# Kernel tuning notes

Measured on AMD Instinct MI355X. Metric: run time of the kernel, lower is better.

Reference implementation:

```python
import jax, jax.numpy as jnp
import numpy as np
from jax import lax

K = 5          # kernel_size
P = K // 2     # padding
DN = ('NCHW', 'OIHW', 'NCHW')


def _dwconv(z, wt, bt):
    # depthwise conv: z [b,c,h,w], wt [c,1,K,K], bt [c]
    c = z.shape[1]
    y = lax.conv_general_dilated(z, wt, (1, 1), [(P, P), (P, P)],
                                 feature_group_count=c, dimension_numbers=DN)
    return y + bt[None, :, None, None]


def setup_inputs() -> dict:
    key = jax.random.key(0)
    ks = jax.random.split(key, 8)
    b, c, h, w = 8, 64, 256, 256
    return {
        'x': jax.random.normal(ks[0], (b, c, h, w), jnp.float32),
        'w1': jax.random.normal(ks[1], (3, c, 1, K, K), jnp.float32) * 0.1,
        'b1': jax.random.normal(ks[2], (3, c), jnp.float32) * 0.1,
        'w2': jax.random.normal(ks[3], (3, c, 1, K, K), jnp.float32) * 0.1,
        'b2': jax.random.normal(ks[4], (3, c), jnp.float32) * 0.1,
        'wk': jax.random.normal(ks[5], (K * K * c, c), jnp.float32) * 0.1,
        'bk': jax.random.normal(ks[6], (K * K * c,), jnp.float32) * 0.1,
        'bias': jnp.zeros((c,), jnp.float32),
    }


def reference(x, w1, b1, w2, b2, wk, bk, bias):
    b, c, h, w = x.shape
    # avgpool 2x2 stride 2
    t = x.reshape(b, c, h // 2, 2, w // 2, 2).mean(axis=(3, 5))
    # Block1: 3 depthwise convs
    for i in range(3):
        t = _dwconv(t, w1[i], b1[i])
    # maxpool 2x2 stride 2
    hh, ww = t.shape[2], t.shape[3]
    t = t.reshape(b, c, hh // 2, 2, ww // 2, 2).max(axis=(3, 5))
    # Block2: 3 depthwise convs
    for i in range(3):
        t = _dwconv(t, w2[i], b2[i])
    # adaptive avg pool to 1x1 -> [b, c]
    g = t.mean(axis=(2, 3))
    # tokernel 1x1 conv -> per-sample depthwise kernels [b*c, 1, K, K]
    kern = (jnp.einsum('bc,oc->bo', g, wk) + bk).reshape(b * c, 1, K, K)
    # per-sample dynamic depthwise conv (groups = b*c)
    y = lax.conv_general_dilated(x.reshape(1, b * c, h, w), kern, (1, 1),
                                 [(P, P), (P, P)], feature_group_count=b * c,
                                 dimension_numbers=DN)
    return y.reshape(b, c, h, w) + bias[None, :, None, None]
```

## Files before the change

### kernel.cpp

```cpp
#include <hip/hip_runtime.h>

#define BB 8
#define CC 64
#define HH 256
#define WW 256
#define H1 128
#define W1 128
#define KK 5

template<int SS>
__device__ __forceinline__ void conv4x4(const float* __restrict__ src,
                                        const float* __restrict__ wr,
                                        float bv, float a[4][4])
{
#pragma unroll
    for (int i = 0; i < 4; i++)
#pragma unroll
        for (int j = 0; j < 4; j++) a[i][j] = bv;
#pragma unroll
    for (int ir = 0; ir < 8; ir++) {
        const float* s = src + ir * SS;
        float4 L = *(const float4*)s;
        float4 R = *(const float4*)(s + 4);
        float e[8] = {L.x, L.y, L.z, L.w, R.x, R.y, R.z, R.w};
#pragma unroll
        for (int i = 0; i < 4; i++) {
            const int ky = ir - i;
            if (ky >= 0 && ky < 5) {
#pragma unroll
                for (int kx = 0; kx < 5; kx++) {
                    const float wv = wr[ky * 5 + kx];
#pragma unroll
                    for (int j = 0; j < 4; j++) a[i][j] += e[j + kx] * wv;
                }
            }
        }
    }
}

__global__ __launch_bounds__(512, 4) void k_block1(
    const float* __restrict__ x, const float* __restrict__ w1,
    const float* __restrict__ b1, float* __restrict__ t1)
{
    const int plane = blockIdx.z;
    const int c = plane & 63;
    const int tx = blockIdx.x, ty = blockIdx.y;
    const int tid = threadIdx.x;

    __shared__ __align__(16) float sA[76 * 76];
    __shared__ __align__(16) float sB[72 * 76];

    const float* xp = x + (size_t)plane * HH * WW;
    const int row0 = ty * 64 - 6, col0 = tx * 64 - 6;

    for (int i = tid; i < 76 * 38; i += 512) {
        int r = i / 38, j = i % 38;
        int gr = row0 + r;
        int xc = 2 * col0 + 4 * j;
        float4 t0 = make_float4(0.f, 0.f, 0.f, 0.f);
        float4 t1v = make_float4(0.f, 0.f, 0.f, 0.f);
        if ((unsigned)gr < H1 && (unsigned)xc < WW) {
            t0  = *(const float4*)(xp + (size_t)(2 * gr) * WW + xc);
            t1v = *(const float4*)(xp + (size_t)(2 * gr + 1) * WW + xc);
        }
        float p0 = 0.25f * (t0.x + t0.y + t1v.x + t1v.y);
        float p1 = 0.25f * (t0.z + t0.w + t1v.z + t1v.w);
        *(float2*)&sA[r * 76 + 2 * j] = make_float2(p0, p1);
    }
    __syncthreads();

    {
        float wr[25];
#pragma unroll
        for (int k = 0; k < 25; k++) wr[k] = w1[0 * CC * 25 + c * 25 + k];
        const float bv = b1[0 * CC + c];
        if (tid < 324) {
            int tr = (tid / 18) * 4, tc = (tid % 18) * 4;
            float a[4][4];
            conv4x4<76>(&sA[tr * 76 + tc], wr, bv, a);
#pragma unroll
            for (int i = 0; i < 4; i++) {
                int gor = ty * 64 - 4 + tr + i;
                bool rok = (unsigned)gor < H1;
#pragma unroll
                for (int j = 0; j < 4; j++) {
                    int goc = tx * 64 - 4 + tc + j;
                    if (!(rok && (unsigned)goc < W1)) a[i][j] = 0.f;
                }
                *(float4*)&sB[(tr + i) * 76 + tc] =
                    make_float4(a[i][0], a[i][1], a[i][2], a[i][3]);
            }
        }
    }
    __syncthreads();

    {
        float wr[25];
#pragma unroll
        for (int k = 0; k < 25; k++) wr[k] = w1[1 * CC * 25 + c * 25 + k];
        const float bv = b1[1 * CC + c];
        if (tid < 289) {
            int tr = (tid / 17) * 4, tc = (tid % 17) * 4;
            float a[4][4];
            conv4x4<76>(&sB[tr * 76 + tc], wr, bv, a);
#pragma unroll
            for (int i = 0; i < 4; i++) {
                int gor = ty * 64 - 2 + tr + i;
                bool rok = (unsigned)gor < H1;
#pragma unroll
                for (int j = 0; j < 4; j++) {
                    int goc = tx * 64 - 2 + tc + j;
                    if (!(rok && (unsigned)goc < W1)) a[i][j] = 0.f;
                }
                *(float4*)&sA[(tr + i) * 68 + tc] =
                    make_float4(a[i][0], a[i][1], a[i][2], a[i][3]);
            }
        }
    }
    __syncthreads();

    {
        float wr[25];
#pragma unroll
        for (int k = 0; k < 25; k++) wr[k] = w1[2 * CC * 25 + c * 25 + k];
        const float bv = b1[2 * CC + c];
        float* tp = t1 + (size_t)plane * H1 * W1;
        const int tr = (tid / 16) * 2, tc = (tid % 16) * 4;
        float a[2][4];
#pragma unroll
        for (int i = 0; i < 2; i++)
#pragma unroll
            for (int j = 0; j < 4; j++) a[i][j] = bv;
#pragma unroll
        for (int ir = 0; ir < 6; ir++) {
            const float* s = &sA[(tr + ir) * 68 + tc];
            float4 L = *(const float4*)s;
            float4 R = *(const float4*)(s + 4);
            float e[8] = {L.x, L.y, L.z, L.w, R.x, R.y, R.z, R.w};
#pragma unroll
            for (int i = 0; i < 2; i++) {
                const int ky = ir - i;
                if (ky >= 0 && ky < 5) {
#pragma unroll
                    for (int kx = 0; kx < 5; kx++) {
                        const float wv = wr[ky * 5 + kx];
#pragma unroll
                        for (int j = 0; j < 4; j++) a[i][j] += e[j + kx] * wv;
                    }
                }
            }
        }
#pragma unroll
        for (int i = 0; i < 2; i++)
            *(float4*)&tp[(size_t)(ty * 64 + tr + i) * W1 + tx * 64 + tc] =
                make_float4(a[i][0], a[i][1], a[i][2], a[i][3]);
    }
}

__global__ __launch_bounds__(512, 4) void k_block2(
    const float* __restrict__ t1, const float* __restrict__ w2,
    const float* __restrict__ b2, float* __restrict__ g)
{
    const int plane = blockIdx.x;
    const int c = plane & 63;
    const int tid = threadIdx.x;

    __shared__ __align__(16) float sA[68 * 68];
    __shared__ __align__(16) float sB[68 * 68];
    __shared__ float red[8];

    const float* tp = t1 + (size_t)plane * H1 * W1;
    for (int i = tid; i < 68 * 68; i += 512) {
        int r = i / 68, cc2 = i % 68;
        float v = 0.f;
        if (r >= 2 && r < 66 && cc2 >= 2 && cc2 < 66) {
            const float2 a0 = *(const float2*)(tp + (size_t)(2 * (r - 2)) * W1 + 2 * (cc2 - 2));
            const float2 a1 = *(const float2*)(tp + (size_t)(2 * (r - 2) + 1) * W1 + 2 * (cc2 - 2));
            v = fmaxf(fmaxf(a0.x, a0.y), fmaxf(a1.x, a1.y));
        }
        sA[i] = v;
        sB[i] = 0.f;
    }
    __syncthreads();

    const int tr = (tid / 16) * 2, tc = (tid % 16) * 4;
#pragma unroll
    for (int cv = 0; cv < 3; cv++) {
        const float* src = (cv & 1) ? sB : sA;
        float* dst = (cv & 1) ? sA : sB;
        float wr[25];
#pragma unroll
        for (int k = 0; k < 25; k++) wr[k] = w2[cv * CC * 25 + c * 25 + k];
        const float bv = b2[cv * CC + c];
        float a[2][4];
#pragma unroll
        for (int i = 0; i < 2; i++)
#pragma unroll
            for (int j = 0; j < 4; j++) a[i][j] = bv;
#pragma unroll
        for (int ir = 0; ir < 6; ir++) {
            const float* s = &src[(tr + ir) * 68 + tc];
            float4 L = *(const float4*)s;
            float4 R = *(const float4*)(s + 4);
            float e[8] = {L.x, L.y, L.z, L.w, R.x, R.y, R.z, R.w};
#pragma unroll
            for (int i = 0; i < 2; i++) {
                const int ky = ir - i;
                if (ky >= 0 && ky < 5) {
#pragma unroll
                    for (int kx = 0; kx < 5; kx++) {
                        const float wv = wr[ky * 5 + kx];
#pragma unroll
                        for (int j = 0; j < 4; j++) a[i][j] += e[j + kx] * wv;
                    }
                }
            }
        }
#pragma unroll
        for (int i = 0; i < 2; i++) {
            float2* d = (float2*)&dst[(tr + i + 2) * 68 + tc + 2];
            d[0] = make_float2(a[i][0], a[i][1]);
            d[1] = make_float2(a[i][2], a[i][3]);
        }
        __syncthreads();
    }

    float s = 0.f;
    for (int i = tid; i < 64 * 64; i += 512) {
        int r = i >> 6, cc2 = i & 63;
        s += sB[(r + 2) * 68 + 2 + cc2];
    }
#pragma unroll
    for (int off = 32; off > 0; off >>= 1) s += __shfl_down(s, off);
    if ((tid & 63) == 0) red[tid >> 6] = s;
    __syncthreads();
    if (tid == 0) {
        float t = 0.f;
#pragma unroll
        for (int k = 0; k < 8; k++) t += red[k];
        g[plane] = t * (1.f / 4096.f);
    }
}

__global__ __launch_bounds__(256) void k_kern(
    const float* __restrict__ g, const float* __restrict__ wk,
    const float* __restrict__ bk, float* __restrict__ kern)
{
    const int o = blockIdx.x * 256 + threadIdx.x;
    const int b = o / 1600, oo = o - b * 1600;
    float v = bk[oo];
    const float* wp = wk + (size_t)oo * 64;
    const float* gp = g + b * 64;
#pragma unroll 16
    for (int k = 0; k < 64; k++) v += gp[k] * wp[k];
    kern[o] = v;
}

__global__ __launch_bounds__(256) void k_dyn(
    const float* __restrict__ x, const float* __restrict__ kern,
    const float* __restrict__ bias, float* __restrict__ out)
{
    const int plane = blockIdx.z;
    const int tx = blockIdx.x, ty = blockIdx.y;
    const int tid = threadIdx.x;

    __shared__ __align__(16) float sx[68 * 76];

    const float* xp = x + (size_t)plane * HH * WW;
    const int R0 = ty * 64, C0 = tx * 64;

#pragma unroll
    for (int k = 0; k < 5; k++) {
        int i = tid + k * 256;
        if (i < 68 * 18) {
            int r = i / 18, q = i - r * 18;
            int gr = R0 - 2 + r;
            int gc = C0 - 4 + 4 * q;
            float4 v = make_float4(0.f, 0.f, 0.f, 0.f);
            if ((unsigned)gr < HH && (unsigned)gc < WW)
                v = *(const float4*)(xp + (size_t)gr * WW + gc);
            *(float4*)&sx[r * 76 + 4 * q] = v;
        }
    }

    float w[25];
#pragma unroll
    for (int k = 0; k < 25; k++) w[k] = kern[(size_t)plane * 25 + k];
    const float bv = bias[plane & 63];

    __syncthreads();

    const int tr = (tid >> 4) * 4;
    const int tc = (tid & 15) * 4;
    float acc[4][4];
#pragma unroll
    for (int i = 0; i < 4; i++)
#pragma unroll
        for (int j = 0; j < 4; j++) acc[i][j] = bv;

#pragma unroll
    for (int ir = 0; ir < 8; ir++) {
        const float* s = &sx[(tr + ir) * 76 + tc];
        float4 A = *(const float4*)s;
        float4 B4 = *(const float4*)(s + 4);
        float4 Cv = *(const float4*)(s + 8);
        float e[12] = {A.x, A.y, A.z, A.w, B4.x, B4.y, B4.z, B4.w,
                       Cv.x, Cv.y, Cv.z, Cv.w};
#pragma unroll
        for (int i = 0; i < 4; i++) {
            const int ky = ir - i;
            if (ky >= 0 && ky < 5) {
#pragma unroll
                for (int kx = 0; kx < 5; kx++) {
                    const float wv = w[ky * 5 + kx];
#pragma unroll
                    for (int j = 0; j < 4; j++) acc[i][j] += e[j + kx + 2] * wv;
                }
            }
        }
    }

    float* op = out + (size_t)plane * HH * WW + (size_t)(R0 + tr) * WW + C0 + tc;
#pragma unroll
    for (int i = 0; i < 4; i++)
        *(float4*)(op + (size_t)i * WW) = make_float4(acc[i][0], acc[i][1], acc[i][2], acc[i][3]);
}

extern "C" void kernel_launch(void* const* d_in, const int* in_sizes, int n_in,
                              void* d_out, int out_size, void* d_ws, size_t ws_size,
                              hipStream_t stream)
{
    const float* x    = (const float*)d_in[0];
    const float* w1   = (const float*)d_in[1];
    const float* b1   = (const float*)d_in[2];
    const float* w2   = (const float*)d_in[3];
    const float* b2   = (const float*)d_in[4];
    const float* wk   = (const float*)d_in[5];
    const float* bk   = (const float*)d_in[6];
    const float* bias = (const float*)d_in[7];
    float* out = (float*)d_out;

    float* ws   = (float*)d_ws;
    float* t1   = ws;
    float* g    = ws + 8388608;
    float* kern = g + 512;

    k_block1<<<dim3(2, 2, 512), 512, 0, stream>>>(x, w1, b1, t1);
    k_block2<<<dim3(512), 512, 0, stream>>>(t1, w2, b2, g);
    k_kern<<<dim3(50), 256, 0, stream>>>(g, wk, bk, kern);
    k_dyn<<<dim3(4, 4, 512), 256, 0, stream>>>(x, kern, bias, out);
}
```

Before: 131.1 us.

## Fuse block1 and block2 into one per-plane kernel using shared memory

Merges the avgpool, three block-1 depthwise convs, maxpool, three block-2 convs and the global mean into a single kernel with one 1024-thread workgroup per plane. The whole 128x128 pooled plane stays in LDS, so the t1 intermediate no longer goes to global memory, one launch is dropped, and the overlapping-halo recompute between tiles disappears. The cost is about 139 KB of LDS per workgroup, which allows only one workgroup per CU, and only 512 workgroups in total, so occupancy and parallelism are much lower.

```diff
diff --git a/kernel.cpp b/kernel.cpp
--- a/kernel.cpp
+++ b/kernel.cpp
@@ -38,197 +38,136 @@
     }
 }
 
-__global__ __launch_bounds__(512, 4) void k_block1(
+template<int SS>
+__device__ __forceinline__ void conv1x4(const float* __restrict__ src,
+                                        const float* __restrict__ wr,
+                                        float bv, float a[4])
+{
+#pragma unroll
+    for (int j = 0; j < 4; j++) a[j] = bv;
+#pragma unroll
+    for (int ir = 0; ir < 5; ir++) {
+        const float* s = src + ir * SS;
+        float4 L = *(const float4*)s;
+        float4 R = *(const float4*)(s + 4);
+        float e[8] = {L.x, L.y, L.z, L.w, R.x, R.y, R.z, R.w};
+#pragma unroll
+        for (int kx = 0; kx < 5; kx++) {
+            const float wv = wr[ir * 5 + kx];
+#pragma unroll
+            for (int j = 0; j < 4; j++) a[j] += e[j + kx] * wv;
+        }
+    }
+}
+
+__global__ __launch_bounds__(1024, 4) void k_block12(
     const float* __restrict__ x, const float* __restrict__ w1,
-    const float* __restrict__ b1, float* __restrict__ t1)
-{
-    const int plane = blockIdx.z;
-    const int c = plane & 63;
-    const int tx = blockIdx.x, ty = blockIdx.y;
-    const int tid = threadIdx.x;
-
-    __shared__ __align__(16) float sA[76 * 76];
-    __shared__ __align__(16) float sB[72 * 76];
-
-    const float* xp = x + (size_t)plane * HH * WW;
-    const int row0 = ty * 64 - 6, col0 = tx * 64 - 6;
-
-    for (int i = tid; i < 76 * 38; i += 512) {
-        int r = i / 38, j = i % 38;
-        int gr = row0 + r;
-        int xc = 2 * col0 + 4 * j;
-        float4 t0 = make_float4(0.f, 0.f, 0.f, 0.f);
-        float4 t1v = make_float4(0.f, 0.f, 0.f, 0.f);
-        if ((unsigned)gr < H1 && (unsigned)xc < WW) {
-            t0  = *(const float4*)(xp + (size_t)(2 * gr) * WW + xc);
-            t1v = *(const float4*)(xp + (size_t)(2 * gr + 1) * WW + xc);
-        }
-        float p0 = 0.25f * (t0.x + t0.y + t1v.x + t1v.y);
-        float p1 = 0.25f * (t0.z + t0.w + t1v.z + t1v.w);
-        *(float2*)&sA[r * 76 + 2 * j] = make_float2(p0, p1);
-    }
-    __syncthreads();
-
-    {
-        float wr[25];
-#pragma unroll
-        for (int k = 0; k < 25; k++) wr[k] = w1[0 * CC * 25 + c * 25 + k];
-        const float bv = b1[0 * CC + c];
-        if (tid < 324) {
-            int tr = (tid / 18) * 4, tc = (tid % 18) * 4;
-            float a[4][4];
-            conv4x4<76>(&sA[tr * 76 + tc], wr, bv, a);
-#pragma unroll
-            for (int i = 0; i < 4; i++) {
-                int gor = ty * 64 - 4 + tr + i;
-                bool rok = (unsigned)gor < H1;
-#pragma unroll
-                for (int j = 0; j < 4; j++) {
-                    int goc = tx * 64 - 4 + tc + j;
-                    if (!(rok && (unsigned)goc < W1)) a[i][j] = 0.f;
-                }
-                *(float4*)&sB[(tr + i) * 76 + tc] =
-                    make_float4(a[i][0], a[i][1], a[i][2], a[i][3]);
-            }
-        }
-    }
-    __syncthreads();
-
-    {
-        float wr[25];
-#pragma unroll
-        for (int k = 0; k < 25; k++) wr[k] = w1[1 * CC * 25 + c * 25 + k];
-        const float bv = b1[1 * CC + c];
-        if (tid < 289) {
-            int tr = (tid / 17) * 4, tc = (tid % 17) * 4;
-            float a[4][4];
-            conv4x4<76>(&sB[tr * 76 + tc], wr, bv, a);
-#pragma unroll
-            for (int i = 0; i < 4; i++) {
-                int gor = ty * 64 - 2 + tr + i;
-                bool rok = (unsigned)gor < H1;
-#pragma unroll
-                for (int j = 0; j < 4; j++) {
-                    int goc = tx * 64 - 2 + tc + j;
-                    if (!(rok && (unsigned)goc < W1)) a[i][j] = 0.f;
-                }
-                *(float4*)&sA[(tr + i) * 68 + tc] =
-                    make_float4(a[i][0], a[i][1], a[i][2], a[i][3]);
-            }
-        }
-    }
-    __syncthreads();
-
-    {
-        float wr[25];
-#pragma unroll
-        for (int k = 0; k < 25; k++) wr[k] = w1[2 * CC * 25 + c * 25 + k];
-        const float bv = b1[2 * CC + c];
-        float* tp = t1 + (size_t)plane * H1 * W1;
-        const int tr = (tid / 16) * 2, tc = (tid % 16) * 4;
-        float a[2][4];
-#pragma unroll
-        for (int i = 0; i < 2; i++)
-#pragma unroll
-            for (int j = 0; j < 4; j++) a[i][j] = bv;
-#pragma unroll
-        for (int ir = 0; ir < 6; ir++) {
-            const float* s = &sA[(tr + ir) * 68 + tc];
-            float4 L = *(const float4*)s;
-            float4 R = *(const float4*)(s + 4);
-            float e[8] = {L.x, L.y, L.z, L.w, R.x, R.y, R.z, R.w};
-#pragma unroll
-            for (int i = 0; i < 2; i++) {
-                const int ky = ir - i;
-                if (ky >= 0 && ky < 5) {
-#pragma unroll
-                    for (int kx = 0; kx < 5; kx++) {
-                        const float wv = wr[ky * 5 + kx];
-#pragma unroll
-                        for (int j = 0; j < 4; j++) a[i][j] += e[j + kx] * wv;
-                    }
-                }
-            }
-        }
-#pragma unroll
-        for (int i = 0; i < 2; i++)
-            *(float4*)&tp[(size_t)(ty * 64 + tr + i) * W1 + tx * 64 + tc] =
-                make_float4(a[i][0], a[i][1], a[i][2], a[i][3]);
-    }
-}
-
-__global__ __launch_bounds__(512, 4) void k_block2(
-    const float* __restrict__ t1, const float* __restrict__ w2,
+    const float* __restrict__ b1, const float* __restrict__ w2,
     const float* __restrict__ b2, float* __restrict__ g)
 {
     const int plane = blockIdx.x;
     const int c = plane & 63;
     const int tid = threadIdx.x;
 
-    __shared__ __align__(16) float sA[68 * 68];
-    __shared__ __align__(16) float sB[68 * 68];
-    __shared__ float red[8];
-
-    const float* tp = t1 + (size_t)plane * H1 * W1;
-    for (int i = tid; i < 68 * 68; i += 512) {
-        int r = i / 68, cc2 = i % 68;
+    __shared__ __align__(16) float sA[132 * 132];
+    __shared__ __align__(16) float sB[132 * 132];
+    __shared__ float red[16];
+
+    const float* xp = x + (size_t)plane * HH * WW;
+
+#pragma unroll
+    for (int k = 0; k < 5; k++) {
+        int i = tid + k * 1024;
+        if (i < 132 * 132 / 4)
+            ((float4*)sB)[i] = make_float4(0.f, 0.f, 0.f, 0.f);
+    }
+
+#pragma unroll
+    for (int k = 0; k < 9; k++) {
+        int i = tid + k * 1024;
+        if (i < 132 * 66) {
+            int r = i / 66, c2 = i % 66;
+            float2 v = make_float2(0.f, 0.f);
+            if (r >= 2 && r < 130 && c2 >= 1 && c2 <= 64) {
+                int pr = r - 2;
+                int xc = 4 * c2 - 4;
+                float4 a0 = *(const float4*)(xp + (size_t)(2 * pr) * WW + xc);
+                float4 a1 = *(const float4*)(xp + (size_t)(2 * pr + 1) * WW + xc);
+                v.x = 0.25f * (a0.x + a0.y + a1.x + a1.y);
+                v.y = 0.25f * (a0.z + a0.w + a1.z + a1.w);
+            }
+            *(float2*)&sA[r * 132 + 2 * c2] = v;
+        }
+    }
+    __syncthreads();
+
+    {
+        const int tr = (tid >> 5) * 4, tc = (tid & 31) * 4;
+#pragma unroll
+        for (int cv = 0; cv < 3; cv++) {
+            const float* src = (cv & 1) ? sB : sA;
+            float* dst = (cv & 1) ? sA : sB;
+            float wr[25];
+#pragma unroll
+            for (int k = 0; k < 25; k++) wr[k] = w1[cv * CC * 25 + c * 25 + k];
+            const float bv = b1[cv * CC + c];
+            float a[4][4];
+            conv4x4<132>(&src[tr * 132 + tc], wr, bv, a);
+#pragma unroll
+            for (int i = 0; i < 4; i++) {
+                float2* d = (float2*)&dst[(tr + i + 2) * 132 + tc + 2];
+                d[0] = make_float2(a[i][0], a[i][1]);
+                d[1] = make_float2(a[i][2], a[i][3]);
+            }
+            __syncthreads();
+        }
+    }
+
+    float* pB = sA;
+    float* pC = sA + 5440;
+    for (int i = tid; i < 68 * 76; i += 1024) {
+        int r = i / 76, cc2 = i % 76;
         float v = 0.f;
         if (r >= 2 && r < 66 && cc2 >= 2 && cc2 < 66) {
-            const float2 a0 = *(const float2*)(tp + (size_t)(2 * (r - 2)) * W1 + 2 * (cc2 - 2));
-            const float2 a1 = *(const float2*)(tp + (size_t)(2 * (r - 2) + 1) * W1 + 2 * (cc2 - 2));
-            v = fmaxf(fmaxf(a0.x, a0.y), fmaxf(a1.x, a1.y));
-        }
-        sA[i] = v;
-        sB[i] = 0.f;
-    }
-    __syncthreads();
-
-    const int tr = (tid / 16) * 2, tc = (tid % 16) * 4;
-#pragma unroll
-    for (int cv = 0; cv < 3; cv++) {
-        const float* src = (cv & 1) ? sB : sA;
-        float* dst = (cv & 1) ? sA : sB;
+            const float* p = &sB[(size_t)(2 * (r - 2) + 2) * 132 + 2 * (cc2 - 2) + 2];
+            v = fmaxf(fmaxf(p[0], p[1]), fmaxf(p[132], p[133]));
+        }
+        pB[i] = v;
+        pC[i] = 0.f;
+    }
+    __syncthreads();
+
+    const int r = tid >> 4, c0 = (tid & 15) * 4;
+    {
         float wr[25];
 #pragma unroll
-        for (int k = 0; k < 25; k++) wr[k] = w2[cv * CC * 25 + c * 25 + k];
-        const float bv = b2[cv * CC + c];
-        float a[2][4];
-#pragma unroll
-        for (int i = 0; i < 2; i++)
-#pragma unroll
-            for (int j = 0; j < 4; j++) a[i][j] = bv;
-#pragma unroll
-        for (int ir = 0; ir < 6; ir++) {
-            const float* s = &src[(tr + ir) * 68 + tc];
-            float4 L = *(const float4*)s;
-            float4 R = *(const float4*)(s + 4);
-            float e[8] = {L.x, L.y, L.z, L.w, R.x, R.y, R.z, R.w};
-#pragma unroll
-            for (int i = 0; i < 2; i++) {
-                const int ky = ir - i;
-                if (ky >= 0 && ky < 5) {
-#pragma unroll
-                    for (int kx = 0; kx < 5; kx++) {
-                        const float wv = wr[ky * 5 + kx];
-#pragma unroll
-                        for (int j = 0; j < 4; j++) a[i][j] += e[j + kx] * wv;
-                    }
-                }
-            }
-        }
-#pragma unroll
-        for (int i = 0; i < 2; i++) {
-            float2* d = (float2*)&dst[(tr + i + 2) * 68 + tc + 2];
-            d[0] = make_float2(a[i][0], a[i][1]);
-            d[1] = make_float2(a[i][2], a[i][3]);
-        }
-        __syncthreads();
-    }
-
-    float s = 0.f;
-    for (int i = tid; i < 64 * 64; i += 512) {
-        int r = i >> 6, cc2 = i & 63;
-        s += sB[(r + 2) * 68 + 2 + cc2];
+        for (int k = 0; k < 25; k++) wr[k] = w2[0 * CC * 25 + c * 25 + k];
+        float a[4];
+        conv1x4<76>(&pB[r * 76 + c0], wr, b2[0 * CC + c], a);
+        float2* d = (float2*)&pC[(r + 2) * 76 + c0 + 2];
+        d[0] = make_float2(a[0], a[1]);
+        d[1] = make_float2(a[2], a[3]);
+    }
+    __syncthreads();
+    {
+        float wr[25];
+#pragma unroll
+        for (int k = 0; k < 25; k++) wr[k] = w2[1 * CC * 25 + c * 25 + k];
+        float a[4];
+        conv1x4<76>(&pC[r * 76 + c0], wr, b2[1 * CC + c], a);
+        float2* d = (float2*)&pB[(r + 2) * 76 + c0 + 2];
+        d[0] = make_float2(a[0], a[1]);
+        d[1] = make_float2(a[2], a[3]);
+    }
+    __syncthreads();
+    float s;
+    {
+        float wr[25];
+#pragma unroll
+        for (int k = 0; k < 25; k++) wr[k] = w2[2 * CC * 25 + c * 25 + k];
+        float a[4];
+        conv1x4<76>(&pB[r * 76 + c0], wr, b2[2 * CC + c], a);
+        s = a[0] + a[1] + a[2] + a[3];
     }
 #pragma unroll
     for (int off = 32; off > 0; off >>= 1) s += __shfl_down(s, off);
@@ -237,7 +176,7 @@
     if (tid == 0) {
         float t = 0.f;
 #pragma unroll
-        for (int k = 0; k < 8; k++) t += red[k];
+        for (int k = 0; k < 16; k++) t += red[k];
         g[plane] = t * (1.f / 4096.f);
     }
 }
@@ -341,12 +280,10 @@
     float* out = (float*)d_out;
 
     float* ws   = (float*)d_ws;
-    float* t1   = ws;
-    float* g    = ws + 8388608;
-    float* kern = g + 512;
-
-    k_block1<<<dim3(2, 2, 512), 512, 0, stream>>>(x, w1, b1, t1);
-    k_block2<<<dim3(512), 512, 0, stream>>>(t1, w2, b2, g);
+    float* g    = ws;
+    float* kern = ws + 512;
+
+    k_block12<<<dim3(512), 1024, 0, stream>>>(x, w1, b1, w2, b2, g);
     k_kern<<<dim3(50), 256, 0, stream>>>(g, wk, bk, kern);
     k_dyn<<<dim3(4, 4, 512), 256, 0, stream>>>(x, kern, bias, out);
 }
```

After: 121.4 us. -7.4%, faster.
